# Optimization experiments

Measured on AMD Instinct MI355X. Metric: run time of the kernel, lower is better.

Reference implementation:

```python
import jax, jax.numpy as jnp
import numpy as np

EXPERT_ID = 3
NUM_EXPERTS = 8
FULL_DIM = 4096
EXPERT_DIM = 1024
SLICE = FULL_DIM // NUM_EXPERTS          # 512
S0 = EXPERT_ID * SLICE
S1 = S0 + SLICE
FP_MIN = EXPERT_ID / NUM_EXPERTS         # 0.375
FP_MAX = (EXPERT_ID + 1) / NUM_EXPERTS   # 0.5
GATE_HID = SLICE // 4                    # 128


def _xavier(key, shape):
    fan_out, fan_in = shape
    lim = float(np.sqrt(6.0 / (fan_in + fan_out)))
    return jax.random.uniform(key, shape, minval=-lim, maxval=lim, dtype=jnp.float32)


def setup_inputs() -> dict:
    key = jax.random.key(0)
    ks = jax.random.split(key, 9)
    B, P = 4, 4096
    tokens = jax.random.normal(ks[0], (B, P, FULL_DIM), dtype=jnp.float32)
    fingerprints = jax.random.uniform(ks[1], (P,), dtype=jnp.float32)
    # learned params (torch nn.Linear stores weight as [out, in])
    gate_w1 = _xavier(ks[2], (GATE_HID, SLICE))
    gate_b1 = jnp.zeros((GATE_HID,), dtype=jnp.float32)
    gate_w2 = _xavier(ks[3], (1, GATE_HID))
    gate_b2 = jnp.zeros((1,), dtype=jnp.float32)
    wq = _xavier(ks[4], (EXPERT_DIM, SLICE))
    wk = _xavier(ks[5], (EXPERT_DIM, SLICE))
    wv = _xavier(ks[6], (EXPERT_DIM, SLICE))
    penta = jax.random.normal(ks[7], (5, EXPERT_DIM), dtype=jnp.float32) * 0.02
    penta = penta / jnp.linalg.norm(penta, axis=-1, keepdims=True)  # _init_weights normalizes
    alpha = jnp.asarray(1.0, dtype=jnp.float32)
    return {
        'tokens': tokens, 'fingerprints': fingerprints, 'alpha': alpha,
        'gate_w1': gate_w1, 'gate_b1': gate_b1, 'gate_w2': gate_w2, 'gate_b2': gate_b2,
        'wq': wq, 'wk': wk, 'wv': wv, 'pentachoron': penta,
    }


def reference(tokens, fingerprints, alpha, gate_w1, gate_b1, gate_w2, gate_b2,
              wq, wk, wv, pentachoron):
    # expert 3 is not the last expert -> strict upper bound
    mask = (fingerprints >= FP_MIN) & (fingerprints < FP_MAX)        # [P] bool
    # gather selected patches, then slice this expert's feature band
    my_features = tokens[..., S0:S1][:, mask]                        # [B, p, SLICE]
    # gating MLP: Linear -> GELU(exact) -> Linear -> Sigmoid
    h = jax.nn.gelu(my_features @ gate_w1.T + gate_b1, approximate=False)
    alpha_gate = jax.nn.sigmoid(h @ gate_w2.T + gate_b2)             # [B, p, 1]
    alpha_weight = jax.nn.sigmoid(alpha)
    my_features = my_features * (alpha_gate * alpha_weight + (1.0 - alpha_weight))
    Q = my_features @ wq.T                                           # [B, p, D]
    K = my_features @ wk.T
    V = my_features @ wv.T
    # per-vertex affinities, vectorized over the 5 pentachoron vertices
    dirs = pentachoron / jnp.linalg.norm(pentachoron, axis=-1, keepdims=True)
    K_aff = jnp.einsum('bpd,vd->vbp', K, dirs)                       # [5, B, p]
    Q_aff = jnp.einsum('bpd,vd->vbp', Q, dirs)
    return (Q, K, V, K_aff, Q_aff, mask)
```

## Files before the change

### kernel.cpp

```cpp
#include <hip/hip_runtime.h>
#include <hip/hip_bf16.h>

#define FULL_DIM 4096
#define EXPERT_DIM 1024
#define SLICE 512
#define S0 (3*SLICE)
#define GATE_HID 128
#define P_TOK 4096
#define BATCH 4
#define NCONV 1600
#define NCW 16

typedef __bf16 bf16;
typedef __bf16 bf16x4 __attribute__((ext_vector_type(4)));
typedef __bf16 bf16x8 __attribute__((ext_vector_type(8)));
typedef float f32x4 __attribute__((ext_vector_type(4)));

__device__ inline void gl_lds16(const void* g, void* l) {
    __builtin_amdgcn_global_load_lds((const __attribute__((address_space(1))) void*)g,
                                     (__attribute__((address_space(3))) void*)l, 16, 0, 0);
}

__global__ void k_setup(const float* __restrict__ wq, const float* __restrict__ wk,
                        const float* __restrict__ wv, const float* __restrict__ gw1,
                        const float* __restrict__ penta, const float* __restrict__ fp,
                        bf16* __restrict__ wqkvb, bf16* __restrict__ w1b,
                        float* __restrict__ cwp, float* __restrict__ mask_out,
                        int* __restrict__ idx) {
    __shared__ float sd[5][64];
    __shared__ float red[5][4];
    __shared__ int offs[256];
    const int bid = blockIdx.x, t = threadIdx.x;
    if (bid < NCONV) {
        int i = bid * 1024 + t * 4;
        if (i < 3 * 524288) {
            const float* src = (i < 524288) ? wq : (i < 2 * 524288 ? wk : wv);
            float4 v = *(const float4*)(src + (i & 524287));
            bf16x4 b = { (bf16)v.x, (bf16)v.y, (bf16)v.z, (bf16)v.w };
            *(bf16x4*)(wqkvb + i) = b;
        } else {
            int j = i - 3 * 524288;
            float4 v = *(const float4*)(gw1 + j);
            bf16x4 b = { (bf16)v.x, (bf16)v.y, (bf16)v.z, (bf16)v.w };
            *(bf16x4*)(w1b + j) = b;
        }
        return;
    }
    if (bid == NCONV) {
        int base = t * 16;
        unsigned bits = 0;
        int c = 0;
#pragma unroll
        for (int i = 0; i < 16; i++) {
            float v = fp[base + i];
            bool m = (v >= 0.375f) && (v < 0.5f);
            mask_out[base + i] = m ? 1.0f : 0.0f;
            bits |= ((unsigned)m) << i;
            c += (int)m;
        }
        offs[t] = c;
        __syncthreads();
        if (t == 0) {
            int s = 0;
            for (int i = 0; i < 256; i++) { int cc = offs[i]; offs[i] = s; s += cc; }
        }
        __syncthreads();
        int o = offs[t];
#pragma unroll
        for (int i = 0; i < 16; i++)
            if (bits & (1u << i)) idx[o++] = base + i;
        return;
    }
    {
        const int cb = bid - (NCONV + 1);
        const int d0 = cb * 64;
        const int lane = t & 63, wave = t >> 6;
#pragma unroll
        for (int v = 0; v < 5; v++) {
            float s = 0.f;
#pragma unroll
            for (int i = 0; i < 4; i++) { float x = penta[v * 1024 + t + i * 256]; s += x * x; }
            for (int d = 32; d; d >>= 1) s += __shfl_xor(s, d);
            if (lane == 0) red[v][wave] = s;
        }
        __syncthreads();
        for (int e = t; e < 5 * 64; e += 256) {
            int v = e >> 6, dd = e & 63;
            float inv = rsqrtf(red[v][0] + red[v][1] + red[v][2] + red[v][3]);
            sd[v][dd] = penta[v * 1024 + d0 + dd] * inv;
        }
        __syncthreads();
#pragma unroll
        for (int pass = 0; pass < 2; pass++) {
            int col = pass * 256 + t;
            float aK[5] = {0, 0, 0, 0, 0}, aQ[5] = {0, 0, 0, 0, 0};
            for (int d = 0; d < 64; d += 4) {
#pragma unroll
                for (int u = 0; u < 4; u++) {
                    float kv = wk[(size_t)(d0 + d + u) * 512 + col];
                    float qv = wq[(size_t)(d0 + d + u) * 512 + col];
                    float dv;
#pragma unroll
                    for (int v = 0; v < 5; v++) {
                        dv = sd[v][d + u];
                        aK[v] += dv * kv;
                        aQ[v] += dv * qv;
                    }
                }
            }
#pragma unroll
            for (int v = 0; v < 5; v++) {
                cwp[((size_t)cb * 10 + v) * 512 + col] = aK[v];
                cwp[((size_t)cb * 10 + 5 + v) * 512 + col] = aQ[v];
            }
        }
    }
}

__launch_bounds__(256)
__global__ void k_gate(const float* __restrict__ tokens, const int* __restrict__ idx,
                       const bf16* __restrict__ w1b, const float* __restrict__ gb1,
                       const float* __restrict__ gw2, const float* __restrict__ gb2,
                       const float* __restrict__ alpha, int p, int M,
                       bf16* __restrict__ Fs) {
    __shared__ bf16 F[32][520];
    __shared__ bf16 W1[128][72];
    __shared__ float H[32][132];
    __shared__ int trow[32];
    __shared__ float scl[32];
    const int t = threadIdx.x, wave = t >> 6, lane = t & 63;
    const int fr = lane & 15, fq = lane >> 4;
    const int m0 = blockIdx.x * 32;

    if (t < 32) {
        int m = m0 + t;
        int r = -1;
        if (m < M) { int b = m / p; int j = m - b * p; r = b * P_TOK + idx[j]; }
        trow[t] = r;
    }
    __syncthreads();
#pragma unroll
    for (int it = 0; it < 16; it++) {
        int r = it * 2 + (t >> 7);
        int c4 = (t & 127) * 4;
        int tr = trow[r];
        float4 v = {0.f, 0.f, 0.f, 0.f};
        if (tr >= 0) v = *(const float4*)(tokens + (size_t)tr * FULL_DIM + S0 + c4);
        bf16x4 b = { (bf16)v.x, (bf16)v.y, (bf16)v.z, (bf16)v.w };
        *(bf16x4*)(&F[r][c4]) = b;
    }
    __syncthreads();
    f32x4 acc[2][2];
#pragma unroll
    for (int i = 0; i < 2; i++)
#pragma unroll
        for (int j = 0; j < 2; j++) acc[i][j] = (f32x4){0.f, 0.f, 0.f, 0.f};
    for (int k0 = 0; k0 < 512; k0 += 64) {
        {
            int n = t >> 1, ch = (t & 1) * 32;
            const bf16* src = w1b + (size_t)n * 512 + k0 + ch;
#pragma unroll
            for (int q = 0; q < 4; q++)
                *(bf16x8*)(&W1[n][ch + q * 8]) = *(const bf16x8*)(src + q * 8);
        }
        __syncthreads();
#pragma unroll
        for (int ks = 0; ks < 2; ks++) {
            bf16x8 a0 = *(const bf16x8*)(&F[fr][k0 + ks * 32 + fq * 8]);
            bf16x8 a1 = *(const bf16x8*)(&F[16 + fr][k0 + ks * 32 + fq * 8]);
            bf16x8 b0 = *(const bf16x8*)(&W1[wave * 32 + fr][ks * 32 + fq * 8]);
            bf16x8 b1 = *(const bf16x8*)(&W1[wave * 32 + 16 + fr][ks * 32 + fq * 8]);
            acc[0][0] = __builtin_amdgcn_mfma_f32_16x16x32_bf16(a0, b0, acc[0][0], 0, 0, 0);
            acc[0][1] = __builtin_amdgcn_mfma_f32_16x16x32_bf16(a0, b1, acc[0][1], 0, 0, 0);
            acc[1][0] = __builtin_amdgcn_mfma_f32_16x16x32_bf16(a1, b0, acc[1][0], 0, 0, 0);
            acc[1][1] = __builtin_amdgcn_mfma_f32_16x16x32_bf16(a1, b1, acc[1][1], 0, 0, 0);
        }
        __syncthreads();
    }
#pragma unroll
    for (int mi = 0; mi < 2; mi++)
#pragma unroll
        for (int ni = 0; ni < 2; ni++) {
            int col = wave * 32 + ni * 16 + fr;
            float bias = gb1[col];
#pragma unroll
            for (int r = 0; r < 4; r++) {
                int row = mi * 16 + fq * 4 + r;
                float v = acc[mi][ni][r] + bias;
                H[row][col] = 0.5f * v * (1.0f + erff(v * 0.70710678118f));
            }
        }
    __syncthreads();
    {
        int r = wave * 8 + (lane >> 3), g = lane & 7;
        float s = 0.f;
#pragma unroll
        for (int i = 0; i < 16; i++) { int c = g + i * 8; s += H[r][c] * gw2[c]; }
        s += __shfl_xor(s, 1); s += __shfl_xor(s, 2); s += __shfl_xor(s, 4);
        if (g == 0) {
            float aw = 1.0f / (1.0f + expf(-alpha[0]));
            float gt = 1.0f / (1.0f + expf(-(s + gb2[0])));
            scl[r] = gt * aw + (1.0f - aw);
        }
    }
    __syncthreads();
#pragma unroll
    for (int it = 0; it < 16; it++) {
        int r = it * 2 + (t >> 7);
        int c4 = (t & 127) * 4;
        bf16x4 b = *(const bf16x4*)(&F[r][c4]);
        float sc = scl[r];
        bf16x4 o = { (bf16)((float)b[0] * sc), (bf16)((float)b[1] * sc),
                     (bf16)((float)b[2] * sc), (bf16)((float)b[3] * sc) };
        *(bf16x4*)(Fs + (size_t)(m0 + r) * 512 + c4) = o;
    }
}

__launch_bounds__(256)
__global__ void k_qkv(const bf16* __restrict__ A, const bf16* __restrict__ W,
                      const float* __restrict__ cwp, float* __restrict__ out,
                      float* __restrict__ aff, int M) {
    __shared__ bf16 As[2][128 * 32];
    __shared__ bf16 Bs[2][128 * 32];
    const int t = threadIdx.x, wave = t >> 6, lane = t & 63;
    const int fr = lane & 15, fq = lane >> 4;

    if (blockIdx.y == 24) {
        bf16* cwt = (bf16*)As;
        for (int e = t; e < 16 * 512; e += 256) {
            int v = e >> 9, c = e & 511;
            float s = 0.f;
            if (v < 10) {
#pragma unroll
                for (int cb = 0; cb < NCW; cb++)
                    s += cwp[((size_t)cb * 10 + v) * 512 + c];
            }
            int byte = v * 1024 + ((((c >> 3) ^ (v & 7)) << 4)) + (c & 7) * 2;
            *(bf16*)((char*)cwt + byte) = (bf16)s;
        }
        __syncthreads();
        const int m0w = blockIdx.x * 128 + wave * 32;
        f32x4 acc0 = (f32x4){0.f, 0.f, 0.f, 0.f};
        f32x4 acc1 = (f32x4){0.f, 0.f, 0.f, 0.f};
        for (int k0 = 0; k0 < 512; k0 += 32) {
            int chunk = (k0 >> 3) + fq;
            bf16x8 b = *(const bf16x8*)((char*)cwt + fr * 1024 + ((chunk ^ (fr & 7)) << 4));
            bf16x8 a0 = *(const bf16x8*)(A + (size_t)(m0w + fr) * 512 + k0 + fq * 8);
            bf16x8 a1 = *(const bf16x8*)(A + (size_t)(m0w + 16 + fr) * 512 + k0 + fq * 8);
            acc0 = __builtin_amdgcn_mfma_f32_16x16x32_bf16(a0, b, acc0, 0, 0, 0);
            acc1 = __builtin_amdgcn_mfma_f32_16x16x32_bf16(a1, b, acc1, 0, 0, 0);
        }
        if (fr < 10) {
#pragma unroll
            for (int r = 0; r < 4; r++) {
                int m = m0w + fq * 4 + r;
                if (m < M) aff[(size_t)fr * M + m] = acc0[r];
                m += 16;
                if (m < M) aff[(size_t)fr * M + m] = acc1[r];
            }
        }
        return;
    }

    const int m0 = blockIdx.x * 128, n0 = blockIdx.y * 128;
    const int wr = wave >> 1, wc = wave & 1;

    f32x4 acc[4][4];
#pragma unroll
    for (int i = 0; i < 4; i++)
#pragma unroll
        for (int j = 0; j < 4; j++) acc[i][j] = (f32x4){0.f, 0.f, 0.f, 0.f};

    const bf16* ga = A + (size_t)(m0 + (t >> 2)) * 512 + (t & 3) * 8;
    const bf16* gb = W + (size_t)(n0 + (t >> 2)) * 512 + (t & 3) * 8;

#define STAGE(buf, ko)                                              \
    gl_lds16(ga + (ko),            &As[buf][wave * 512]);           \
    gl_lds16(ga + (ko) + 64 * 512, &As[buf][2048 + wave * 512]);    \
    gl_lds16(gb + (ko),            &Bs[buf][wave * 512]);           \
    gl_lds16(gb + (ko) + 64 * 512, &Bs[buf][2048 + wave * 512]);

    STAGE(0, 0);
    __syncthreads();
    int cur = 0;
    for (int kt = 0; kt < 16; kt++) {
        if (kt < 15) { STAGE(cur ^ 1, (kt + 1) * 32); }
        bf16x8 af[4], bw[4];
#pragma unroll
        for (int mi = 0; mi < 4; mi++)
            af[mi] = *(const bf16x8*)(&As[cur][(wr * 64 + mi * 16 + fr) * 32 + fq * 8]);
#pragma unroll
        for (int ni = 0; ni < 4; ni++)
            bw[ni] = *(const bf16x8*)(&Bs[cur][(wc * 64 + ni * 16 + fr) * 32 + fq * 8]);
#pragma unroll
        for (int mi = 0; mi < 4; mi++)
#pragma unroll
            for (int ni = 0; ni < 4; ni++)
                acc[mi][ni] = __builtin_amdgcn_mfma_f32_16x16x32_bf16(af[mi], bw[ni], acc[mi][ni], 0, 0, 0);
        __syncthreads();
        cur ^= 1;
    }
#undef STAGE

    const int z = blockIdx.y >> 3;
    const int nb = (blockIdx.y & 7) * 128;
    float* obase = out + (size_t)z * M * EXPERT_DIM;
#pragma unroll
    for (int mi = 0; mi < 4; mi++)
#pragma unroll
        for (int ni = 0; ni < 4; ni++) {
            int col = nb + wc * 64 + ni * 16 + fr;
#pragma unroll
            for (int r = 0; r < 4; r++) {
                int row = m0 + wr * 64 + mi * 16 + fq * 4 + r;
                if (row < M) obase[(size_t)row * EXPERT_DIM + col] = acc[mi][ni][r];
            }
        }
}

extern "C" void kernel_launch(void* const* d_in, const int* in_sizes, int n_in,
                              void* d_out, int out_size, void* d_ws, size_t ws_size,
                              hipStream_t stream) {
    const float* tokens = (const float*)d_in[0];
    const float* fps    = (const float*)d_in[1];
    const float* alpha  = (const float*)d_in[2];
    const float* gw1    = (const float*)d_in[3];
    const float* gb1    = (const float*)d_in[4];
    const float* gw2    = (const float*)d_in[5];
    const float* gb2    = (const float*)d_in[6];
    const float* wq     = (const float*)d_in[7];
    const float* wk     = (const float*)d_in[8];
    const float* wv     = (const float*)d_in[9];
    const float* penta  = (const float*)d_in[10];
    float* out = (float*)d_out;

    int p = (out_size - P_TOK) / (3 * BATCH * EXPERT_DIM + 2 * 5 * BATCH);
    if (p <= 0) return;
    int M = BATCH * p;
    int Mpad = (M + 127) & ~127;

    char* ws = (char*)d_ws;
    size_t off = 0;
    int*   idx   = (int*)(ws + off);   off += 16 * 1024;
    bf16*  wqkvb = (bf16*)(ws + off);  off += (size_t)3 * EXPERT_DIM * SLICE * 2;
    bf16*  w1b   = (bf16*)(ws + off);  off += (size_t)GATE_HID * SLICE * 2;
    float* cwp   = (float*)(ws + off); off += (size_t)NCW * 10 * 512 * 4;
    bf16*  Fs    = (bf16*)(ws + off);  off += (size_t)Mpad * SLICE * 2;
    (void)ws_size;

    float* aff_out  = out + (size_t)3 * M * EXPERT_DIM;
    float* mask_out = aff_out + (size_t)10 * M;

    k_setup<<<NCONV + 1 + NCW, 256, 0, stream>>>(wq, wk, wv, gw1, penta, fps,
                                                 wqkvb, w1b, cwp, mask_out, idx);
    k_gate<<<Mpad / 32, 256, 0, stream>>>(tokens, idx, w1b, gb1, gw2, gb2, alpha, p, M, Fs);
    k_qkv<<<dim3(Mpad / 128, 25), 256, 0, stream>>>(Fs, wqkvb, cwp, out, aff_out, M);
}
```

Measured before the change: 59.61 us.

## Fuse setup and gating into one front kernel, enlarge QKV GEMM tiles

```diff
diff --git a/kernel.cpp b/kernel.cpp
--- a/kernel.cpp
+++ b/kernel.cpp
@@ -8,7 +8,7 @@
 #define GATE_HID 128
 #define P_TOK 4096
 #define BATCH 4
-#define NCONV 1600
+#define NCONV 1536
 #define NCW 16
 
 typedef __bf16 bf16;
@@ -21,60 +21,169 @@
                                      (__attribute__((address_space(3))) void*)l, 16, 0, 0);
 }
 
-__global__ void k_setup(const float* __restrict__ wq, const float* __restrict__ wk,
-                        const float* __restrict__ wv, const float* __restrict__ gw1,
-                        const float* __restrict__ penta, const float* __restrict__ fp,
-                        bf16* __restrict__ wqkvb, bf16* __restrict__ w1b,
-                        float* __restrict__ cwp, float* __restrict__ mask_out,
-                        int* __restrict__ idx) {
+__launch_bounds__(256)
+__global__ void k_front(const float* __restrict__ tokens, const float* __restrict__ fp,
+                        const float* __restrict__ alpha,
+                        const float* __restrict__ gw1, const float* __restrict__ gb1,
+                        const float* __restrict__ gw2, const float* __restrict__ gb2,
+                        const float* __restrict__ wq, const float* __restrict__ wk,
+                        const float* __restrict__ wv, const float* __restrict__ penta,
+                        bf16* __restrict__ wqkvb, float* __restrict__ cwp,
+                        float* __restrict__ mask_out, bf16* __restrict__ Fs,
+                        int p, int M, int ngate) {
+    __shared__ bf16 F[32][520];
+    __shared__ union { bf16 W1[128][72]; float H[32][132]; } u;
+    __shared__ int trow[32];
+    __shared__ float scl[32];
+    __shared__ int sOffs[256];
+    __shared__ unsigned short sBits[256];
+    __shared__ int wsum[4];
     __shared__ float sd[5][64];
     __shared__ float red[5][4];
-    __shared__ int offs[256];
     const int bid = blockIdx.x, t = threadIdx.x;
-    if (bid < NCONV) {
-        int i = bid * 1024 + t * 4;
-        if (i < 3 * 524288) {
-            const float* src = (i < 524288) ? wq : (i < 2 * 524288 ? wk : wv);
-            float4 v = *(const float4*)(src + (i & 524287));
+    const int wave = t >> 6, lane = t & 63;
+
+    if (bid < ngate) {
+        const int fr = lane & 15, fq = lane >> 4;
+        const int m0 = bid * 32;
+        {
+            int base = t * 16;
+            unsigned bits = 0;
+            int cnt = 0;
+#pragma unroll
+            for (int i = 0; i < 16; i++) {
+                float v = fp[base + i];
+                bool m = (v >= 0.375f) && (v < 0.5f);
+                bits |= ((unsigned)m) << i;
+                cnt += (int)m;
+            }
+            int incl = cnt;
+#pragma unroll
+            for (int d = 1; d < 64; d <<= 1) {
+                int n = __shfl_up(incl, d);
+                if (lane >= d) incl += n;
+            }
+            if (lane == 63) wsum[wave] = incl;
+            __syncthreads();
+            int wbase = 0;
+            for (int w = 0; w < 4; w++) if (w < wave) wbase += wsum[w];
+            sOffs[t] = wbase + incl - cnt;
+            sBits[t] = (unsigned short)bits;
+        }
+        __syncthreads();
+        if (t < 32) {
+            int m = m0 + t;
+            int r = -1;
+            if (m < M) {
+                int b = m / p, j = m - b * p;
+                int lo = 0, hi = 255;
+                while (lo < hi) { int mid = (lo + hi + 1) >> 1; if (sOffs[mid] <= j) lo = mid; else hi = mid - 1; }
+                int jj = j - sOffs[lo];
+                unsigned bt = sBits[lo];
+                int pos = 0;
+#pragma unroll
+                for (int bit = 0; bit < 16; bit++) {
+                    if ((bt >> bit) & 1) { if (jj == 0) { pos = bit; break; } jj--; }
+                }
+                r = b * P_TOK + lo * 16 + pos;
+            }
+            trow[t] = r;
+        }
+        __syncthreads();
+#pragma unroll
+        for (int it = 0; it < 16; it++) {
+            int r = it * 2 + (t >> 7);
+            int c4 = (t & 127) * 4;
+            int tr = trow[r];
+            float4 v = {0.f, 0.f, 0.f, 0.f};
+            if (tr >= 0) v = *(const float4*)(tokens + (size_t)tr * FULL_DIM + S0 + c4);
             bf16x4 b = { (bf16)v.x, (bf16)v.y, (bf16)v.z, (bf16)v.w };
-            *(bf16x4*)(wqkvb + i) = b;
-        } else {
-            int j = i - 3 * 524288;
-            float4 v = *(const float4*)(gw1 + j);
-            bf16x4 b = { (bf16)v.x, (bf16)v.y, (bf16)v.z, (bf16)v.w };
-            *(bf16x4*)(w1b + j) = b;
+            *(bf16x4*)(&F[r][c4]) = b;
+        }
+        __syncthreads();
+        f32x4 acc[2][2];
+#pragma unroll
+        for (int i = 0; i < 2; i++)
+#pragma unroll
+            for (int j = 0; j < 2; j++) acc[i][j] = (f32x4){0.f, 0.f, 0.f, 0.f};
+        for (int k0 = 0; k0 < 512; k0 += 64) {
+            {
+                int n = t >> 1, ch = (t & 1) * 32;
+                const float* src = gw1 + (size_t)n * 512 + k0 + ch;
+#pragma unroll
+                for (int q = 0; q < 4; q++) {
+                    float4 a = *(const float4*)(src + q * 8);
+                    float4 b = *(const float4*)(src + q * 8 + 4);
+                    bf16x8 w = { (bf16)a.x, (bf16)a.y, (bf16)a.z, (bf16)a.w,
+                                 (bf16)b.x, (bf16)b.y, (bf16)b.z, (bf16)b.w };
+                    *(bf16x8*)(&u.W1[n][ch + q * 8]) = w;
+                }
+            }
+            __syncthreads();
+#pragma unroll
+            for (int ks = 0; ks < 2; ks++) {
+                bf16x8 a0 = *(const bf16x8*)(&F[fr][k0 + ks * 32 + fq * 8]);
+                bf16x8 a1 = *(const bf16x8*)(&F[16 + fr][k0 + ks * 32 + fq * 8]);
+                bf16x8 b0 = *(const bf16x8*)(&u.W1[wave * 32 + fr][ks * 32 + fq * 8]);
+                bf16x8 b1 = *(const bf16x8*)(&u.W1[wave * 32 + 16 + fr][ks * 32 + fq * 8]);
+                acc[0][0] = __builtin_amdgcn_mfma_f32_16x16x32_bf16(a0, b0, acc[0][0], 0, 0, 0);
+                acc[0][1] = __builtin_amdgcn_mfma_f32_16x16x32_bf16(a0, b1, acc[0][1], 0, 0, 0);
+                acc[1][0] = __builtin_amdgcn_mfma_f32_16x16x32_bf16(a1, b0, acc[1][0], 0, 0, 0);
+                acc[1][1] = __builtin_amdgcn_mfma_f32_16x16x32_bf16(a1, b1, acc[1][1], 0, 0, 0);
+            }
+            __syncthreads();
+        }
+#pragma unroll
+        for (int mi = 0; mi < 2; mi++)
+#pragma unroll
+            for (int ni = 0; ni < 2; ni++) {
+                int col = wave * 32 + ni * 16 + fr;
+                float bias = gb1[col];
+#pragma unroll
+                for (int r = 0; r < 4; r++) {
+                    int row = mi * 16 + fq * 4 + r;
+                    float v = acc[mi][ni][r] + bias;
+                    u.H[row][col] = 0.5f * v * (1.0f + erff(v * 0.70710678118f));
+                }
+            }
+        __syncthreads();
+        {
+            int r = wave * 8 + (lane >> 3), g = lane & 7;
+            float s = 0.f;
+#pragma unroll
+            for (int i = 0; i < 16; i++) { int c = g + i * 8; s += u.H[r][c] * gw2[c]; }
+            s += __shfl_xor(s, 1); s += __shfl_xor(s, 2); s += __shfl_xor(s, 4);
+            if (g == 0) {
+                float aw = 1.0f / (1.0f + expf(-alpha[0]));
+                float gt = 1.0f / (1.0f + expf(-(s + gb2[0])));
+                scl[r] = gt * aw + (1.0f - aw);
+            }
+        }
+        __syncthreads();
+#pragma unroll
+        for (int it = 0; it < 16; it++) {
+            int r = it * 2 + (t >> 7);
+            int c4 = (t & 127) * 4;
+            bf16x4 b = *(const bf16x4*)(&F[r][c4]);
+            float sc = scl[r];
+            bf16x4 o = { (bf16)((float)b[0] * sc), (bf16)((float)b[1] * sc),
+                         (bf16)((float)b[2] * sc), (bf16)((float)b[3] * sc) };
+            *(bf16x4*)(Fs + (size_t)(m0 + r) * 512 + c4) = o;
         }
         return;
     }
-    if (bid == NCONV) {
+    if (bid == ngate) {
         int base = t * 16;
-        unsigned bits = 0;
-        int c = 0;
 #pragma unroll
         for (int i = 0; i < 16; i++) {
             float v = fp[base + i];
-            bool m = (v >= 0.375f) && (v < 0.5f);
-            mask_out[base + i] = m ? 1.0f : 0.0f;
-            bits |= ((unsigned)m) << i;
-            c += (int)m;
-        }
-        offs[t] = c;
-        __syncthreads();
-        if (t == 0) {
-            int s = 0;
-            for (int i = 0; i < 256; i++) { int cc = offs[i]; offs[i] = s; s += cc; }
-        }
-        __syncthreads();
-        int o = offs[t];
-#pragma unroll
-        for (int i = 0; i < 16; i++)
-            if (bits & (1u << i)) idx[o++] = base + i;
+            mask_out[base + i] = ((v >= 0.375f) && (v < 0.5f)) ? 1.0f : 0.0f;
+        }
         return;
     }
-    {
-        const int cb = bid - (NCONV + 1);
+    if (bid <= ngate + NCW) {
+        const int cb = bid - (ngate + 1);
         const int d0 = cb * 64;
-        const int lane = t & 63, wave = t >> 6;
 #pragma unroll
         for (int v = 0; v < 5; v++) {
             float s = 0.f;
@@ -96,13 +205,12 @@
             float aK[5] = {0, 0, 0, 0, 0}, aQ[5] = {0, 0, 0, 0, 0};
             for (int d = 0; d < 64; d += 4) {
 #pragma unroll
-                for (int u = 0; u < 4; u++) {
-                    float kv = wk[(size_t)(d0 + d + u) * 512 + col];
-                    float qv = wq[(size_t)(d0 + d + u) * 512 + col];
-                    float dv;
+                for (int uu = 0; uu < 4; uu++) {
+                    float kv = wk[(size_t)(d0 + d + uu) * 512 + col];
+                    float qv = wq[(size_t)(d0 + d + uu) * 512 + col];
 #pragma unroll
                     for (int v = 0; v < 5; v++) {
-                        dv = sd[v][d + u];
+                        float dv = sd[v][d + uu];
                         aK[v] += dv * kv;
                         aQ[v] += dv * qv;
                     }
@@ -114,120 +222,30 @@
                 cwp[((size_t)cb * 10 + 5 + v) * 512 + col] = aQ[v];
             }
         }
+        return;
+    }
+    {
+        int ci = bid - (ngate + 1 + NCW);
+        int i = ci * 1024 + t * 4;
+        const float* src = (i < 524288) ? wq : (i < 2 * 524288 ? wk : wv);
+        float4 v = *(const float4*)(src + (i & 524287));
+        bf16x4 b = { (bf16)v.x, (bf16)v.y, (bf16)v.z, (bf16)v.w };
+        *(bf16x4*)(wqkvb + i) = b;
     }
 }
 
-__launch_bounds__(256)
-__global__ void k_gate(const float* __restrict__ tokens, const int* __restrict__ idx,
-                       const bf16* __restrict__ w1b, const float* __restrict__ gb1,
-                       const float* __restrict__ gw2, const float* __restrict__ gb2,
-                       const float* __restrict__ alpha, int p, int M,
-                       bf16* __restrict__ Fs) {
-    __shared__ bf16 F[32][520];
-    __shared__ bf16 W1[128][72];
-    __shared__ float H[32][132];
-    __shared__ int trow[32];
-    __shared__ float scl[32];
-    const int t = threadIdx.x, wave = t >> 6, lane = t & 63;
-    const int fr = lane & 15, fq = lane >> 4;
-    const int m0 = blockIdx.x * 32;
-
-    if (t < 32) {
-        int m = m0 + t;
-        int r = -1;
-        if (m < M) { int b = m / p; int j = m - b * p; r = b * P_TOK + idx[j]; }
-        trow[t] = r;
-    }
-    __syncthreads();
-#pragma unroll
-    for (int it = 0; it < 16; it++) {
-        int r = it * 2 + (t >> 7);
-        int c4 = (t & 127) * 4;
-        int tr = trow[r];
-        float4 v = {0.f, 0.f, 0.f, 0.f};
-        if (tr >= 0) v = *(const float4*)(tokens + (size_t)tr * FULL_DIM + S0 + c4);
-        bf16x4 b = { (bf16)v.x, (bf16)v.y, (bf16)v.z, (bf16)v.w };
-        *(bf16x4*)(&F[r][c4]) = b;
-    }
-    __syncthreads();
-    f32x4 acc[2][2];
-#pragma unroll
-    for (int i = 0; i < 2; i++)
-#pragma unroll
-        for (int j = 0; j < 2; j++) acc[i][j] = (f32x4){0.f, 0.f, 0.f, 0.f};
-    for (int k0 = 0; k0 < 512; k0 += 64) {
-        {
-            int n = t >> 1, ch = (t & 1) * 32;
-            const bf16* src = w1b + (size_t)n * 512 + k0 + ch;
-#pragma unroll
-            for (int q = 0; q < 4; q++)
-                *(bf16x8*)(&W1[n][ch + q * 8]) = *(const bf16x8*)(src + q * 8);
-        }
-        __syncthreads();
-#pragma unroll
-        for (int ks = 0; ks < 2; ks++) {
-            bf16x8 a0 = *(const bf16x8*)(&F[fr][k0 + ks * 32 + fq * 8]);
-            bf16x8 a1 = *(const bf16x8*)(&F[16 + fr][k0 + ks * 32 + fq * 8]);
-            bf16x8 b0 = *(const bf16x8*)(&W1[wave * 32 + fr][ks * 32 + fq * 8]);
-            bf16x8 b1 = *(const bf16x8*)(&W1[wave * 32 + 16 + fr][ks * 32 + fq * 8]);
-            acc[0][0] = __builtin_amdgcn_mfma_f32_16x16x32_bf16(a0, b0, acc[0][0], 0, 0, 0);
-            acc[0][1] = __builtin_amdgcn_mfma_f32_16x16x32_bf16(a0, b1, acc[0][1], 0, 0, 0);
-            acc[1][0] = __builtin_amdgcn_mfma_f32_16x16x32_bf16(a1, b0, acc[1][0], 0, 0, 0);
-            acc[1][1] = __builtin_amdgcn_mfma_f32_16x16x32_bf16(a1, b1, acc[1][1], 0, 0, 0);
-        }
-        __syncthreads();
-    }
-#pragma unroll
-    for (int mi = 0; mi < 2; mi++)
-#pragma unroll
-        for (int ni = 0; ni < 2; ni++) {
-            int col = wave * 32 + ni * 16 + fr;
-            float bias = gb1[col];
-#pragma unroll
-            for (int r = 0; r < 4; r++) {
-                int row = mi * 16 + fq * 4 + r;
-                float v = acc[mi][ni][r] + bias;
-                H[row][col] = 0.5f * v * (1.0f + erff(v * 0.70710678118f));
-            }
-        }
-    __syncthreads();
-    {
-        int r = wave * 8 + (lane >> 3), g = lane & 7;
-        float s = 0.f;
-#pragma unroll
-        for (int i = 0; i < 16; i++) { int c = g + i * 8; s += H[r][c] * gw2[c]; }
-        s += __shfl_xor(s, 1); s += __shfl_xor(s, 2); s += __shfl_xor(s, 4);
-        if (g == 0) {
-            float aw = 1.0f / (1.0f + expf(-alpha[0]));
-            float gt = 1.0f / (1.0f + expf(-(s + gb2[0])));
-            scl[r] = gt * aw + (1.0f - aw);
-        }
-    }
-    __syncthreads();
-#pragma unroll
-    for (int it = 0; it < 16; it++) {
-        int r = it * 2 + (t >> 7);
-        int c4 = (t & 127) * 4;
-        bf16x4 b = *(const bf16x4*)(&F[r][c4]);
-        float sc = scl[r];
-        bf16x4 o = { (bf16)((float)b[0] * sc), (bf16)((float)b[1] * sc),
-                     (bf16)((float)b[2] * sc), (bf16)((float)b[3] * sc) };
-        *(bf16x4*)(Fs + (size_t)(m0 + r) * 512 + c4) = o;
-    }
-}
-
-__launch_bounds__(256)
+__launch_bounds__(512)
 __global__ void k_qkv(const bf16* __restrict__ A, const bf16* __restrict__ W,
                       const float* __restrict__ cwp, float* __restrict__ out,
                       float* __restrict__ aff, int M) {
-    __shared__ bf16 As[2][128 * 32];
+    __shared__ bf16 As[2][256 * 32];
     __shared__ bf16 Bs[2][128 * 32];
     const int t = threadIdx.x, wave = t >> 6, lane = t & 63;
     const int fr = lane & 15, fq = lane >> 4;
 
     if (blockIdx.y == 24) {
         bf16* cwt = (bf16*)As;
-        for (int e = t; e < 16 * 512; e += 256) {
+        for (int e = t; e < 16 * 512; e += 512) {
             int v = e >> 9, c = e & 511;
             float s = 0.f;
             if (v < 10) {
@@ -239,7 +257,7 @@
             *(bf16*)((char*)cwt + byte) = (bf16)s;
         }
         __syncthreads();
-        const int m0w = blockIdx.x * 128 + wave * 32;
+        const int m0w = blockIdx.x * 256 + wave * 32;
         f32x4 acc0 = (f32x4){0.f, 0.f, 0.f, 0.f};
         f32x4 acc1 = (f32x4){0.f, 0.f, 0.f, 0.f};
         for (int k0 = 0; k0 < 512; k0 += 32) {
@@ -262,7 +280,7 @@
         return;
     }
 
-    const int m0 = blockIdx.x * 128, n0 = blockIdx.y * 128;
+    const int m0 = blockIdx.x * 256, n0 = blockIdx.y * 128;
     const int wr = wave >> 1, wc = wave & 1;
 
     f32x4 acc[4][4];
@@ -274,11 +292,10 @@
     const bf16* ga = A + (size_t)(m0 + (t >> 2)) * 512 + (t & 3) * 8;
     const bf16* gb = W + (size_t)(n0 + (t >> 2)) * 512 + (t & 3) * 8;
 
-#define STAGE(buf, ko)                                              \
-    gl_lds16(ga + (ko),            &As[buf][wave * 512]);           \
-    gl_lds16(ga + (ko) + 64 * 512, &As[buf][2048 + wave * 512]);    \
-    gl_lds16(gb + (ko),            &Bs[buf][wave * 512]);           \
-    gl_lds16(gb + (ko) + 64 * 512, &Bs[buf][2048 + wave * 512]);
+#define STAGE(buf, ko)                                               \
+    gl_lds16(ga + (ko),             &As[buf][wave * 512]);           \
+    gl_lds16(ga + (ko) + 128 * 512, &As[buf][4096 + wave * 512]);    \
+    gl_lds16(gb + (ko),             &Bs[buf][wave * 512]);
 
     STAGE(0, 0);
     __syncthreads();
@@ -337,13 +354,12 @@
     int p = (out_size - P_TOK) / (3 * BATCH * EXPERT_DIM + 2 * 5 * BATCH);
     if (p <= 0) return;
     int M = BATCH * p;
-    int Mpad = (M + 127) & ~127;
+    int Mpad = (M + 255) & ~255;
+    int ngate = Mpad / 32;
 
     char* ws = (char*)d_ws;
     size_t off = 0;
-    int*   idx   = (int*)(ws + off);   off += 16 * 1024;
     bf16*  wqkvb = (bf16*)(ws + off);  off += (size_t)3 * EXPERT_DIM * SLICE * 2;
-    bf16*  w1b   = (bf16*)(ws + off);  off += (size_t)GATE_HID * SLICE * 2;
     float* cwp   = (float*)(ws + off); off += (size_t)NCW * 10 * 512 * 4;
     bf16*  Fs    = (bf16*)(ws + off);  off += (size_t)Mpad * SLICE * 2;
     (void)ws_size;
@@ -351,8 +367,8 @@
     float* aff_out  = out + (size_t)3 * M * EXPERT_DIM;
     float* mask_out = aff_out + (size_t)10 * M;
 
-    k_setup<<<NCONV + 1 + NCW, 256, 0, stream>>>(wq, wk, wv, gw1, penta, fps,
-                                                 wqkvb, w1b, cwp, mask_out, idx);
-    k_gate<<<Mpad / 32, 256, 0, stream>>>(tokens, idx, w1b, gb1, gw2, gb2, alpha, p, M, Fs);
-    k_qkv<<<dim3(Mpad / 128, 25), 256, 0, stream>>>(Fs, wqkvb, cwp, out, aff_out, M);
+    k_front<<<ngate + 1 + NCW + NCONV, 256, 0, stream>>>(
+        tokens, fps, alpha, gw1, gb1, gw2, gb2, wq, wk, wv, penta,
+        wqkvb, cwp, mask_out, Fs, p, M, ngate);
+    k_qkv<<<dim3(Mpad / 256, 25), 512, 0, stream>>>(Fs, wqkvb, cwp, out, aff_out, M);
 }
```

Measured after the change: 49.59 us. 16.8% less time.
